# Kernel tuning notes

Hardware: AMD Instinct MI355X
Metric: run time of the kernel (lower is better)

The kernel has to match this reference:

```python
import jax, jax.numpy as jnp
import numpy as np

APP_DIM = 27
FEA_PE = 6
VIEW_PE = 6
FEATURE_C = 128
DENSITY_SHIFT = -10.0
DISTANCE_SCALE = 25.0
IN_MLPC = 2 * VIEW_PE * 3 + 2 * FEA_PE * APP_DIM + 3 + APP_DIM  # 390


def positional_encoding(x, freqs):
    # x: [..., C] -> [..., 2*freqs*C]
    freq_bands = (2.0 ** jnp.arange(freqs)).astype(x.dtype)
    pts = (x[..., None] * freq_bands).reshape(x.shape[:-1] + (freqs * x.shape[-1],))
    return jnp.concatenate([jnp.sin(pts), jnp.cos(pts)], axis=-1)


def alpha2weights(alpha):
    # alpha: [N_rays, N_samples]; last sample forced opaque (as in source)
    alpha = alpha.at[:, -1].set(1.0)
    trans = jnp.concatenate(
        [jnp.ones((alpha.shape[0], 1), alpha.dtype), 1.0 - alpha + 1e-10], axis=-1)
    T = jnp.cumprod(trans, axis=-1)
    weights = alpha * T[:, :-1]
    return weights, T


def setup_inputs() -> dict:
    key = jax.random.key(0)
    ks = jax.random.split(key, 12)
    N_rays, N_samples = 4096, 128
    sigma_feat = jax.random.normal(ks[0], (N_rays, N_samples), jnp.float32)
    app_features = 0.1 * jax.random.normal(ks[1], (N_rays, N_samples, APP_DIM), jnp.float32)
    vd = jax.random.normal(ks[2], (N_rays, N_samples, 3), jnp.float32)
    viewdirs = vd / (jnp.linalg.norm(vd, axis=-1, keepdims=True) + 1e-8)
    dists = 0.02 * jax.random.uniform(ks[3], (N_rays, N_samples), jnp.float32)

    def linear(k, fan_in, fan_out):
        kw, kb = jax.random.split(k)
        lim = 1.0 / np.sqrt(fan_in)
        W = jax.random.uniform(kw, (fan_in, fan_out), jnp.float32, -lim, lim)
        b = jax.random.uniform(kb, (fan_out,), jnp.float32, -lim, lim)
        return W, b

    W1, b1 = linear(ks[4], IN_MLPC, FEATURE_C)
    W2, b2 = linear(ks[5], FEATURE_C, FEATURE_C)
    W3, _ = linear(ks[6], FEATURE_C, 3)
    b3 = jnp.zeros((3,), jnp.float32)  # bias of last layer initialized to 0 in source
    return {"sigma_feat": sigma_feat, "app_features": app_features,
            "viewdirs": viewdirs, "dists": dists,
            "W1": W1, "b1": b1, "W2": W2, "b2": b2, "W3": W3, "b3": b3}


def reference(sigma_feat, app_features, viewdirs, dists, W1, b1, W2, b2, W3, b3):
    # feature2density: softplus with density_shift
    sigma = jax.nn.softplus(sigma_feat + DENSITY_SHIFT)
    alpha = 1.0 - jnp.exp(-sigma * dists * DISTANCE_SCALE)  # [N_rays, N_samples]
    weights, _T = alpha2weights(alpha)

    # MLPRender_Fea: cat[features, viewdirs, PE(features), PE(viewdirs)]
    mlp_in = jnp.concatenate(
        [app_features, viewdirs,
         positional_encoding(app_features, FEA_PE),
         positional_encoding(viewdirs, VIEW_PE)], axis=-1)  # [R, S, 390]
    h = jax.nn.relu(jnp.einsum('rsc,cf->rsf', mlp_in, W1) + b1)
    h = jax.nn.relu(jnp.einsum('rsf,fg->rsg', h, W2) + b2)
    rgb = jax.nn.sigmoid(jnp.einsum('rsg,go->rso', h, W3) + b3)  # [R, S, 3]

    rgb_map = jnp.sum(weights[..., None] * rgb, axis=-2)  # [R, 3]
    return rgb_map
```

## Files before the change

kernel.cpp:

```cpp
#include <hip/hip_runtime.h>
#include <math.h>

typedef unsigned short u16;
using bf16x8 = __attribute__((ext_vector_type(8))) short;
using f32x4  = __attribute__((ext_vector_type(4))) float;

#define NS      128
#define NBLOCKS 4096
#define KS1     15
#define NSLICE  19

#define POOLSZ 16384

#define BAR() do { asm volatile("s_waitcnt lgkmcnt(0)" ::: "memory");        \
                   __builtin_amdgcn_s_barrier();                              \
                   asm volatile("" ::: "memory"); } while (0)

#define MF(A,B,C) __builtin_amdgcn_mfma_f32_16x16x32_bf16((A),(B),(C),0,0,0)

__device__ __forceinline__ u16 f2bf(float f) {
    unsigned int i = __float_as_uint(f);
    return (u16)((i + 0x7FFFu + ((i >> 16) & 1u)) >> 16);
}

__device__ __forceinline__ unsigned pk(float hi, float lo) {
    unsigned r;
    asm("v_cvt_pk_bf16_f32 %0, %1, %2" : "=v"(r) : "v"(lo), "v"(hi));
    return r;
}
__device__ __forceinline__ u16 f2bf1(float f) {
    return (u16)((__float_as_uint(f) + 0x8000u) >> 16);
}

__device__ __forceinline__ int afoff_h(int m, int k) {
    int chunk = ((k >> 5) * 8 + (m >> 4)) * 64 + ((k >> 3) & 3) * 16 + (m & 15);
    chunk ^= (k >> 3) & 3;
    return chunk * 8 + (k & 7);
}

__device__ __forceinline__ int orig_k(int ch, int slot) {
    if (ch < 27) {
        if (slot == 0) return ch;
        if (slot <= 6) return 30 + ch * 6 + (slot - 1);
        return 192 + ch * 6 + (slot - 7);
    } else {
        int c = ch - 27;
        if (slot == 0) return 27 + c;
        if (slot <= 6) return 354 + c * 6 + (slot - 1);
        return 372 + c * 6 + (slot - 7);
    }
}

__device__ __forceinline__ float ldch(const float* ap, const float* vp, int c) {
    return (c < 27) ? ap[c] : vp[c - 27];
}

__device__ __forceinline__ void build_x(u16* Xb, int m_b, int cl_b, float v) {
    float rev = v * 0.15915494309189535f;
    rev -= floorf(rev);
    float s0 = __builtin_amdgcn_sinf(rev);
    float c0 = __builtin_amdgcn_cosf(rev);
    float s1 = 2.f * s0 * c0, c1 = c0 * c0 - s0 * s0;
    float s2 = 2.f * s1 * c1, c2 = c1 * c1 - s1 * s1;
    float s3 = 2.f * s2 * c2, c3 = c2 * c2 - s2 * s2;
    float s4 = 2.f * s3 * c3, c4 = c3 * c3 - s3 * s3;
    float s5 = 2.f * s4 * c4, c5 = c4 * c4 - s4 * s4;
    uint4 lo, hi;
    lo.x = pk(s0, v);  lo.y = pk(s2, s1);  lo.z = pk(s4, s3);  lo.w = pk(c0, s5);
    hi.x = pk(c2, c1); hi.y = pk(c4, c3);  hi.z = pk(0.f, c5); hi.w = 0u;
    int base = (m_b >> 4) * 512 + ((2 * cl_b) * 16 + (m_b & 15)) * 8;
    *(uint4*)(Xb + base)       = lo;
    *(uint4*)(Xb + base + 128) = hi;
}

__global__ __launch_bounds__(256) void prep_kernel(
    const float* __restrict__ W1, const float* __restrict__ W2,
    const float* __restrict__ W3, u16* __restrict__ ws)
{
    int idx = blockIdx.x * 256 + threadIdx.x;
    if (idx < 61440) {
        int j = idx & 7, lane = (idx >> 3) & 63, nt = (idx >> 9) & 7, ks = idx >> 12;
        int q = lane >> 4, l15 = lane & 15;
        int klocal = q * 8 + j;
        int ch = ks * 2 + (klocal >> 4);
        int slot = klocal & 15;
        int n = nt * 16 + l15;
        ws[idx] = (slot < 13) ? f2bf(W1[orig_k(ch, slot) * 128 + n]) : (u16)0;
    } else if (idx < 77824) {
        int i2 = idx - 61440;
        int j = i2 & 7, lane = (i2 >> 3) & 63, nt = (i2 >> 9) & 7, ks = i2 >> 12;
        int k = ks * 32 + (lane >> 4) * 8 + j;
        int n = nt * 16 + (lane & 15);
        ws[idx] = f2bf(W2[k * 128 + n]);
    } else if (idx < 79872) {
        int i3 = idx - 77824;
        int j = i3 & 7, lane = (i3 >> 3) & 63, ks = i3 >> 9;
        int k = ks * 32 + (lane >> 4) * 8 + j;
        int n = lane & 15;
        ws[idx] = (n < 3) ? f2bf(W3[k * 3 + n]) : (u16)0;
    }
}

#define PHASE(g, BC0,BC1,BC2,BC3, BN0,BN1,BN2,BN3)                            \
  {                                                                           \
    const u16* wpn = wp0 + (2*(g)+2) * 4096;          \
    BN0 = *(const bf16x8*)(wpn);                                              \
    BN1 = *(const bf16x8*)(wpn + 512);                                        \
    BN2 = *(const bf16x8*)(wpn + 4096);                                       \
    BN3 = *(const bf16x8*)(wpn + 4096 + 512);                                 \
    if (4*((g)+2) + cl < 30)                         \
        pv_nxt = ldch(ap, vp, 4*((g)+2) + cl);                                \
    const u16* ab = pool + ((((g)&1) ? 8192 : 0)) + (wm*256 + lane)*8;        \
    bf16x8 a0 = *(const bf16x8*)(ab);                                         \
    bf16x8 a1 = *(const bf16x8*)(ab + 512);                                   \
    bf16x8 a2 = *(const bf16x8*)(ab + 1024);                                  \
    bf16x8 a3 = *(const bf16x8*)(ab + 1536);                                  \
    acc[0][0]=MF(a0,BC0,acc[0][0]); acc[0][1]=MF(a0,BC1,acc[0][1]);           \
    acc[1][0]=MF(a1,BC0,acc[1][0]); acc[1][1]=MF(a1,BC1,acc[1][1]);           \
    acc[2][0]=MF(a2,BC0,acc[2][0]); acc[2][1]=MF(a2,BC1,acc[2][1]);           \
    acc[3][0]=MF(a3,BC0,acc[3][0]); acc[3][1]=MF(a3,BC1,acc[3][1]);           \
    a0 = *(const bf16x8*)(ab + 4096);                                         \
    a1 = *(const bf16x8*)(ab + 4096 + 512);                                   \
    a2 = *(const bf16x8*)(ab + 4096 + 1024);                                  \
    a3 = *(const bf16x8*)(ab + 4096 + 1536);                                  \
    acc[0][0]=MF(a0,BC2,acc[0][0]); acc[0][1]=MF(a0,BC3,acc[0][1]);           \
    acc[1][0]=MF(a1,BC2,acc[1][0]); acc[1][1]=MF(a1,BC3,acc[1][1]);           \
    acc[2][0]=MF(a2,BC2,acc[2][0]); acc[2][1]=MF(a2,BC3,acc[2][1]);           \
    acc[3][0]=MF(a3,BC2,acc[3][0]); acc[3][1]=MF(a3,BC3,acc[3][1]);           \
    if (4*((g)+1) + cl < 30)                             \
        build_x(pool + ((((g)+1)&1) ? 8192 : 0) + (cl>>1)*4096, row, cl&1,    \
                pv_cur);                                                      \
    pv_cur = pv_nxt;                                                          \
    BAR();                                                                    \
  }

__global__ __launch_bounds__(512, 4) void render_kernel(
    const float* __restrict__ sigma_g, const float* __restrict__ app_g,
    const float* __restrict__ view_g,  const float* __restrict__ dists_g,
    const float* __restrict__ b1_g,    const float* __restrict__ b2_g,
    const float* __restrict__ b3_g,    const u16* __restrict__ ws,
    float* __restrict__ out_g)
{
    __shared__ __align__(16) u16 pool[POOLSZ];
    __shared__ __align__(16) float part[NS * 3];
    __shared__ float scanS;
    __shared__ float sum2[6];

    const int tid  = threadIdx.x;
    const int lane = tid & 63;
    const int wave = tid >> 6;
    const int l15  = lane & 15;
    const int quad = lane >> 4;
    const int wm   = wave >> 2;
    const int wn   = wave & 3;

    const int r  = blockIdx.x;
    const int rb = r * NS;
    const int row = tid & 127;
    const int cl  = tid >> 7;
    const float* ap = app_g  + (rb + row) * 27;
    const float* vp = view_g + (rb + row) * 3;

    const u16* wp0 = ws + (wn * 128 + lane) * 8;
    bf16x8 bP0, bP1, bP2, bP3, bQ0, bQ1, bQ2, bQ3;
    bP0 = *(const bf16x8*)(wp0);
    bP1 = *(const bf16x8*)(wp0 + 512);
    bP2 = *(const bf16x8*)(wp0 + 4096);
    bP3 = *(const bf16x8*)(wp0 + 4096 + 512);

    const float b1r0 = b1_g[wn * 32 + l15];
    const float b1r1 = b1_g[wn * 32 + 16 + l15];

    float pv_cur = ldch(ap, vp, cl);
    float pv_nxt = ldch(ap, vp, 4 + cl);

    float alpha = 0.f, prod = 1.f, wr = 0.f;
    if (tid < NS) {
        float x  = sigma_g[rb + tid] - 10.f;
        float sp = (x > 20.f) ? x : log1pf(expf(x));
        alpha = 1.f - expf(-sp * dists_g[rb + tid] * 25.f);
        if (tid == NS - 1) alpha = 1.f;
        float tb = 1.f - alpha + 1e-10f;
        prod = tb;
        #pragma unroll
        for (int d = 1; d < 64; d <<= 1) {
            float v = __shfl_up(prod, d);
            if (lane >= d) prod *= v;
        }
        if (tid == 63) scanS = prod;
    }

    build_x(pool + (cl >> 1) * 4096, row, cl & 1, pv_cur);
    pv_cur = pv_nxt;
    BAR();

    if (tid < NS) {
        float prev = __shfl_up(prod, 1);
        float base = (lane == 0) ? 1.f : prev;
        float scale = (wave == 1) ? scanS : 1.f;
        wr = alpha * base * scale;
    }

    const f32x4 vzero = {0.f, 0.f, 0.f, 0.f};
    f32x4 acc[4][2];
    #pragma unroll
    for (int mt = 0; mt < 4; ++mt)
        #pragma unroll
        for (int nt = 0; nt < 2; ++nt) acc[mt][nt] = vzero;

    #pragma unroll 1
    for (int t = 0; t < 3; ++t) {
        PHASE(2 * t,     bP0, bP1, bP2, bP3, bQ0, bQ1, bQ2, bQ3);
        PHASE(2 * t + 1, bQ0, bQ1, bQ2, bQ3, bP0, bP1, bP2, bP3);
    }
    PHASE(6, bP0, bP1, bP2, bP3, bQ0, bQ1, bQ2, bQ3);

    {
        const u16* wpn = wp0 + 16 * 4096;
        bf16x8 w2a0 = *(const bf16x8*)(wpn);
        bf16x8 w2a1 = *(const bf16x8*)(wpn + 512);
        bf16x8 w2b0 = *(const bf16x8*)(wpn + 4096);
        bf16x8 w2b1 = *(const bf16x8*)(wpn + 4096 + 512);
        bf16x8 w2c0 = *(const bf16x8*)(wpn + 8192);
        bf16x8 w2c1 = *(const bf16x8*)(wpn + 8192 + 512);

        const u16* ab = pool + 8192 + (wm * 256 + lane) * 8;
        bf16x8 a0 = *(const bf16x8*)(ab);
        bf16x8 a1 = *(const bf16x8*)(ab + 512);
        bf16x8 a2 = *(const bf16x8*)(ab + 1024);
        bf16x8 a3 = *(const bf16x8*)(ab + 1536);
        acc[0][0]=MF(a0,bQ0,acc[0][0]); acc[0][1]=MF(a0,bQ1,acc[0][1]);
        acc[1][0]=MF(a1,bQ0,acc[1][0]); acc[1][1]=MF(a1,bQ1,acc[1][1]);
        acc[2][0]=MF(a2,bQ0,acc[2][0]); acc[2][1]=MF(a2,bQ1,acc[2][1]);
        acc[3][0]=MF(a3,bQ0,acc[3][0]); acc[3][1]=MF(a3,bQ1,acc[3][1]);
        BAR();

        #pragma unroll
        for (int mt = 0; mt < 4; ++mt)
            #pragma unroll
            for (int nt = 0; nt < 2; ++nt) {
                int col = wn * 32 + nt * 16 + l15;
                #pragma unroll
                for (int rr = 0; rr < 4; ++rr) {
                    int rw = wm * 64 + mt * 16 + quad * 4 + rr;
                    pool[afoff_h(rw, col)] =
                        f2bf1(fmaxf(acc[mt][nt][rr] + ((nt == 0) ? b1r0 : b1r1), 0.f));
                }
                acc[mt][nt] = vzero;
            }
        BAR();

        #define G2(ks, B0, B1)                                                \
          {                                                                   \
            int cb = ((ks) * 512 + wm * 256 + lane) ^ quad;                   \
            bf16x8 h0 = *(const bf16x8*)(pool + cb * 8);                      \
            bf16x8 h1v = *(const bf16x8*)(pool + (cb + 64) * 8);              \
            bf16x8 h2v = *(const bf16x8*)(pool + (cb + 128) * 8);             \
            bf16x8 h3v = *(const bf16x8*)(pool + (cb + 192) * 8);             \
            acc[0][0]=MF(h0,B0,acc[0][0]); acc[0][1]=MF(h0,B1,acc[0][1]);     \
            acc[1][0]=MF(h1v,B0,acc[1][0]); acc[1][1]=MF(h1v,B1,acc[1][1]);   \
            acc[2][0]=MF(h2v,B0,acc[2][0]); acc[2][1]=MF(h2v,B1,acc[2][1]);   \
            acc[3][0]=MF(h3v,B0,acc[3][0]); acc[3][1]=MF(h3v,B1,acc[3][1]);   \
          }
        G2(0, bQ2, bQ3);
        G2(1, w2a0, w2a1);
        G2(2, w2b0, w2b1);
        G2(3, w2c0, w2c1);
        #undef G2
        BAR();
    }

    const float b2r0 = b2_g[wn * 32 + l15];
    const float b2r1 = b2_g[wn * 32 + 16 + l15];
    #pragma unroll
    for (int mt = 0; mt < 4; ++mt)
        #pragma unroll
        for (int nt = 0; nt < 2; ++nt) {
            int col = wn * 32 + nt * 16 + l15;
            #pragma unroll
            for (int rr = 0; rr < 4; ++rr) {
                int rw = wm * 64 + mt * 16 + quad * 4 + rr;
                pool[afoff_h(rw, col)] =
                    f2bf1(fmaxf(acc[mt][nt][rr] + ((nt == 0) ? b2r0 : b2r1), 0.f));
            }
        }
    BAR();

    const u16* w3r = ws + 77824;
    const float b3v = (l15 < 3) ? b3_g[l15] : 0.f;
    f32x4 acc3 = vzero;
    #pragma unroll
    for (int ks = 0; ks < 4; ++ks) {
        bf16x8 w3f = *(const bf16x8*)(w3r + (ks * 64 + lane) * 8);
        int c = ((ks * 8 + wave) * 64 + lane) ^ quad;
        bf16x8 a3 = *(const bf16x8*)(pool + c * 8);
        acc3 = MF(a3, w3f, acc3);
    }
    if (l15 < 3) {
        #pragma unroll
        for (int rr = 0; rr < 4; ++rr) {
            int rw = wave * 16 + quad * 4 + rr;
            float v = acc3[rr] + b3v;
            part[rw * 3 + l15] = 1.f / (1.f + expf(-v));
        }
    }
    BAR();

    if (tid < NS) {
        float v0 = wr * part[tid * 3 + 0];
        float v1 = wr * part[tid * 3 + 1];
        float v2 = wr * part[tid * 3 + 2];
        #pragma unroll
        for (int d = 1; d < 64; d <<= 1) {
            v0 += __shfl_xor(v0, d);
            v1 += __shfl_xor(v1, d);
            v2 += __shfl_xor(v2, d);
        }
        if (lane == 0) {
            sum2[wave * 3 + 0] = v0;
            sum2[wave * 3 + 1] = v1;
            sum2[wave * 3 + 2] = v2;
        }
    }
    BAR();
    if (tid == 0) {
        out_g[r * 3 + 0] = sum2[0] + sum2[3];
        out_g[r * 3 + 1] = sum2[1] + sum2[4];
        out_g[r * 3 + 2] = sum2[2] + sum2[5];
    }
}

extern "C" void kernel_launch(void* const* d_in, const int* in_sizes, int n_in,
                              void* d_out, int out_size, void* d_ws, size_t ws_size,
                              hipStream_t stream) {
    (void)in_sizes; (void)n_in; (void)out_size; (void)ws_size;
    const float* sigma = (const float*)d_in[0];
    const float* app   = (const float*)d_in[1];
    const float* view  = (const float*)d_in[2];
    const float* dists = (const float*)d_in[3];
    const float* W1    = (const float*)d_in[4];
    const float* b1    = (const float*)d_in[5];
    const float* W2    = (const float*)d_in[6];
    const float* b2    = (const float*)d_in[7];
    const float* W3    = (const float*)d_in[8];
    const float* b3    = (const float*)d_in[9];
    float* out = (float*)d_out;

    u16* ws = (u16*)d_ws;

    prep_kernel<<<312, 256, 0, stream>>>(W1, W2, W3, ws);
    render_kernel<<<NBLOCKS, 512, 0, stream>>>(sigma, app, view, dists,
                                               b1, b2, b3, ws, out);
}
```

Measured before the change: 206.7 us.

## Retile MLP waves to 4x2 grid with triple-buffered weight prefetch and MFMA priority

```diff
diff --git a/kernel.cpp b/kernel.cpp
--- a/kernel.cpp
+++ b/kernel.cpp
@@ -101,36 +101,51 @@
     }
 }
 
-#define PHASE(g, BC0,BC1,BC2,BC3, BN0,BN1,BN2,BN3)                            \
+#define LOADB(N0,N1,N2,N3, s)                                                 \
+    if ((s) < NSLICE) {                                                       \
+        const u16* wp = wp0 + (s) * 4096;                                     \
+        N0 = *(const bf16x8*)(wp);                                            \
+        N1 = *(const bf16x8*)(wp + 512);                                      \
+        N2 = *(const bf16x8*)(wp + 1024);                                     \
+        N3 = *(const bf16x8*)(wp + 1536);                                     \
+    }
+
+#define BODYX(s, C0,C1,C2,C3, N0,N1,N2,N3)                                    \
   {                                                                           \
-    const u16* wpn = wp0 + (2*(g)+2) * 4096;          \
-    BN0 = *(const bf16x8*)(wpn);                                              \
-    BN1 = *(const bf16x8*)(wpn + 512);                                        \
-    BN2 = *(const bf16x8*)(wpn + 4096);                                       \
-    BN3 = *(const bf16x8*)(wpn + 4096 + 512);                                 \
-    if (4*((g)+2) + cl < 30)                         \
-        pv_nxt = ldch(ap, vp, 4*((g)+2) + cl);                                \
-    const u16* ab = pool + ((((g)&1) ? 8192 : 0)) + (wm*256 + lane)*8;        \
+    LOADB(N0,N1,N2,N3, (s)+2);                                                \
+    const u16* ab = pool + ((((s)>>1)&1) ? 8192 : 0) + (((s)&1)*4096)         \
+                    + (wm*128 + lane)*8;                                      \
     bf16x8 a0 = *(const bf16x8*)(ab);                                         \
     bf16x8 a1 = *(const bf16x8*)(ab + 512);                                   \
-    bf16x8 a2 = *(const bf16x8*)(ab + 1024);                                  \
-    bf16x8 a3 = *(const bf16x8*)(ab + 1536);                                  \
-    acc[0][0]=MF(a0,BC0,acc[0][0]); acc[0][1]=MF(a0,BC1,acc[0][1]);           \
-    acc[1][0]=MF(a1,BC0,acc[1][0]); acc[1][1]=MF(a1,BC1,acc[1][1]);           \
-    acc[2][0]=MF(a2,BC0,acc[2][0]); acc[2][1]=MF(a2,BC1,acc[2][1]);           \
-    acc[3][0]=MF(a3,BC0,acc[3][0]); acc[3][1]=MF(a3,BC1,acc[3][1]);           \
-    a0 = *(const bf16x8*)(ab + 4096);                                         \
-    a1 = *(const bf16x8*)(ab + 4096 + 512);                                   \
-    a2 = *(const bf16x8*)(ab + 4096 + 1024);                                  \
-    a3 = *(const bf16x8*)(ab + 4096 + 1536);                                  \
-    acc[0][0]=MF(a0,BC2,acc[0][0]); acc[0][1]=MF(a0,BC3,acc[0][1]);           \
-    acc[1][0]=MF(a1,BC2,acc[1][0]); acc[1][1]=MF(a1,BC3,acc[1][1]);           \
-    acc[2][0]=MF(a2,BC2,acc[2][0]); acc[2][1]=MF(a2,BC3,acc[2][1]);           \
-    acc[3][0]=MF(a3,BC2,acc[3][0]); acc[3][1]=MF(a3,BC3,acc[3][1]);           \
-    if (4*((g)+1) + cl < 30)                             \
+    __builtin_amdgcn_s_setprio(1);                                            \
+    acc[0][0]=MF(a0,C0,acc[0][0]); acc[0][1]=MF(a0,C1,acc[0][1]);             \
+    acc[0][2]=MF(a0,C2,acc[0][2]); acc[0][3]=MF(a0,C3,acc[0][3]);             \
+    acc[1][0]=MF(a1,C0,acc[1][0]); acc[1][1]=MF(a1,C1,acc[1][1]);             \
+    acc[1][2]=MF(a1,C2,acc[1][2]); acc[1][3]=MF(a1,C3,acc[1][3]);             \
+    __builtin_amdgcn_s_setprio(0);                                            \
+  }
+
+#define BODYH(s, C0,C1,C2,C3, N0,N1,N2,N3)                                    \
+  {                                                                           \
+    LOADB(N0,N1,N2,N3, (s)+2);                                                \
+    int cb0 = ((((s)-15)*512) + wm*128 + lane) ^ quad;                        \
+    bf16x8 a0 = *(const bf16x8*)(pool + cb0*8);                               \
+    bf16x8 a1 = *(const bf16x8*)(pool + (cb0+64)*8);                          \
+    __builtin_amdgcn_s_setprio(1);                                            \
+    acc[0][0]=MF(a0,C0,acc[0][0]); acc[0][1]=MF(a0,C1,acc[0][1]);             \
+    acc[0][2]=MF(a0,C2,acc[0][2]); acc[0][3]=MF(a0,C3,acc[0][3]);             \
+    acc[1][0]=MF(a1,C0,acc[1][0]); acc[1][1]=MF(a1,C1,acc[1][1]);             \
+    acc[1][2]=MF(a1,C2,acc[1][2]); acc[1][3]=MF(a1,C3,acc[1][3]);             \
+    __builtin_amdgcn_s_setprio(0);                                            \
+  }
+
+#define GEND(g)                                                               \
+  {                                                                           \
+    if (4*((g)+3) + cl < 30) pv_nxt2 = ldch(ap, vp, 4*((g)+3) + cl);          \
+    if (4*((g)+1) + cl < 30)                                                  \
         build_x(pool + ((((g)+1)&1) ? 8192 : 0) + (cl>>1)*4096, row, cl&1,    \
                 pv_cur);                                                      \
-    pv_cur = pv_nxt;                                                          \
+    pv_cur = pv_nxt; pv_nxt = pv_nxt2;                                        \
     BAR();                                                                    \
   }
 
@@ -151,8 +166,8 @@
     const int wave = tid >> 6;
     const int l15  = lane & 15;
     const int quad = lane >> 4;
-    const int wm   = wave >> 2;
-    const int wn   = wave & 3;
+    const int wm   = wave >> 1;
+    const int wn   = wave & 1;
 
     const int r  = blockIdx.x;
     const int rb = r * NS;
@@ -161,18 +176,18 @@
     const float* ap = app_g  + (rb + row) * 27;
     const float* vp = view_g + (rb + row) * 3;
 
-    const u16* wp0 = ws + (wn * 128 + lane) * 8;
-    bf16x8 bP0, bP1, bP2, bP3, bQ0, bQ1, bQ2, bQ3;
-    bP0 = *(const bf16x8*)(wp0);
-    bP1 = *(const bf16x8*)(wp0 + 512);
-    bP2 = *(const bf16x8*)(wp0 + 4096);
-    bP3 = *(const bf16x8*)(wp0 + 4096 + 512);
-
-    const float b1r0 = b1_g[wn * 32 + l15];
-    const float b1r1 = b1_g[wn * 32 + 16 + l15];
-
-    float pv_cur = ldch(ap, vp, cl);
-    float pv_nxt = ldch(ap, vp, 4 + cl);
+    const u16* wp0 = ws + wn * 2048 + lane * 8;
+    bf16x8 bP0, bP1, bP2, bP3, bQ0, bQ1, bQ2, bQ3, bR0, bR1, bR2, bR3;
+    LOADB(bP0, bP1, bP2, bP3, 0);
+    LOADB(bQ0, bQ1, bQ2, bQ3, 1);
+
+    float b1r[4];
+    #pragma unroll
+    for (int nt = 0; nt < 4; ++nt) b1r[nt] = b1_g[wn * 64 + nt * 16 + l15];
+
+    float pv_cur  = ldch(ap, vp, cl);
+    float pv_nxt  = ldch(ap, vp, 4 + cl);
+    float pv_nxt2 = ldch(ap, vp, 8 + cl);
 
     float alpha = 0.f, prod = 1.f, wr = 0.f;
     if (tid < NS) {
@@ -191,7 +206,7 @@
     }
 
     build_x(pool + (cl >> 1) * 4096, row, cl & 1, pv_cur);
-    pv_cur = pv_nxt;
+    pv_cur = pv_nxt; pv_nxt = pv_nxt2;
     BAR();
 
     if (tid < NS) {
@@ -202,86 +217,63 @@
     }
 
     const f32x4 vzero = {0.f, 0.f, 0.f, 0.f};
-    f32x4 acc[4][2];
-    #pragma unroll
-    for (int mt = 0; mt < 4; ++mt)
-        #pragma unroll
-        for (int nt = 0; nt < 2; ++nt) acc[mt][nt] = vzero;
-
-    #pragma unroll 1
-    for (int t = 0; t < 3; ++t) {
-        PHASE(2 * t,     bP0, bP1, bP2, bP3, bQ0, bQ1, bQ2, bQ3);
-        PHASE(2 * t + 1, bQ0, bQ1, bQ2, bQ3, bP0, bP1, bP2, bP3);
-    }
-    PHASE(6, bP0, bP1, bP2, bP3, bQ0, bQ1, bQ2, bQ3);
-
-    {
-        const u16* wpn = wp0 + 16 * 4096;
-        bf16x8 w2a0 = *(const bf16x8*)(wpn);
-        bf16x8 w2a1 = *(const bf16x8*)(wpn + 512);
-        bf16x8 w2b0 = *(const bf16x8*)(wpn + 4096);
-        bf16x8 w2b1 = *(const bf16x8*)(wpn + 4096 + 512);
-        bf16x8 w2c0 = *(const bf16x8*)(wpn + 8192);
-        bf16x8 w2c1 = *(const bf16x8*)(wpn + 8192 + 512);
-
-        const u16* ab = pool + 8192 + (wm * 256 + lane) * 8;
-        bf16x8 a0 = *(const bf16x8*)(ab);
-        bf16x8 a1 = *(const bf16x8*)(ab + 512);
-        bf16x8 a2 = *(const bf16x8*)(ab + 1024);
-        bf16x8 a3 = *(const bf16x8*)(ab + 1536);
-        acc[0][0]=MF(a0,bQ0,acc[0][0]); acc[0][1]=MF(a0,bQ1,acc[0][1]);
-        acc[1][0]=MF(a1,bQ0,acc[1][0]); acc[1][1]=MF(a1,bQ1,acc[1][1]);
-        acc[2][0]=MF(a2,bQ0,acc[2][0]); acc[2][1]=MF(a2,bQ1,acc[2][1]);
-        acc[3][0]=MF(a3,bQ0,acc[3][0]); acc[3][1]=MF(a3,bQ1,acc[3][1]);
-        BAR();
-
-        #pragma unroll
-        for (int mt = 0; mt < 4; ++mt)
-            #pragma unroll
-            for (int nt = 0; nt < 2; ++nt) {
-                int col = wn * 32 + nt * 16 + l15;
-                #pragma unroll
-                for (int rr = 0; rr < 4; ++rr) {
-                    int rw = wm * 64 + mt * 16 + quad * 4 + rr;
-                    pool[afoff_h(rw, col)] =
-                        f2bf1(fmaxf(acc[mt][nt][rr] + ((nt == 0) ? b1r0 : b1r1), 0.f));
-                }
-                acc[mt][nt] = vzero;
-            }
-        BAR();
-
-        #define G2(ks, B0, B1)                                                \
-          {                                                                   \
-            int cb = ((ks) * 512 + wm * 256 + lane) ^ quad;                   \
-            bf16x8 h0 = *(const bf16x8*)(pool + cb * 8);                      \
-            bf16x8 h1v = *(const bf16x8*)(pool + (cb + 64) * 8);              \
-            bf16x8 h2v = *(const bf16x8*)(pool + (cb + 128) * 8);             \
-            bf16x8 h3v = *(const bf16x8*)(pool + (cb + 192) * 8);             \
-            acc[0][0]=MF(h0,B0,acc[0][0]); acc[0][1]=MF(h0,B1,acc[0][1]);     \
-            acc[1][0]=MF(h1v,B0,acc[1][0]); acc[1][1]=MF(h1v,B1,acc[1][1]);   \
-            acc[2][0]=MF(h2v,B0,acc[2][0]); acc[2][1]=MF(h2v,B1,acc[2][1]);   \
-            acc[3][0]=MF(h3v,B0,acc[3][0]); acc[3][1]=MF(h3v,B1,acc[3][1]);   \
-          }
-        G2(0, bQ2, bQ3);
-        G2(1, w2a0, w2a1);
-        G2(2, w2b0, w2b1);
-        G2(3, w2c0, w2c1);
-        #undef G2
-        BAR();
-    }
-
-    const float b2r0 = b2_g[wn * 32 + l15];
-    const float b2r1 = b2_g[wn * 32 + 16 + l15];
-    #pragma unroll
-    for (int mt = 0; mt < 4; ++mt)
-        #pragma unroll
-        for (int nt = 0; nt < 2; ++nt) {
-            int col = wn * 32 + nt * 16 + l15;
+    f32x4 acc[2][4];
+    #pragma unroll
+    for (int mt = 0; mt < 2; ++mt)
+        #pragma unroll
+        for (int nt = 0; nt < 4; ++nt) acc[mt][nt] = vzero;
+
+    BODYX(0,  bP0,bP1,bP2,bP3, bR0,bR1,bR2,bR3);
+    BODYX(1,  bQ0,bQ1,bQ2,bQ3, bP0,bP1,bP2,bP3);  GEND(0);
+    BODYX(2,  bR0,bR1,bR2,bR3, bQ0,bQ1,bQ2,bQ3);
+    BODYX(3,  bP0,bP1,bP2,bP3, bR0,bR1,bR2,bR3);  GEND(1);
+    BODYX(4,  bQ0,bQ1,bQ2,bQ3, bP0,bP1,bP2,bP3);
+    BODYX(5,  bR0,bR1,bR2,bR3, bQ0,bQ1,bQ2,bQ3);  GEND(2);
+    BODYX(6,  bP0,bP1,bP2,bP3, bR0,bR1,bR2,bR3);
+    BODYX(7,  bQ0,bQ1,bQ2,bQ3, bP0,bP1,bP2,bP3);  GEND(3);
+    BODYX(8,  bR0,bR1,bR2,bR3, bQ0,bQ1,bQ2,bQ3);
+    BODYX(9,  bP0,bP1,bP2,bP3, bR0,bR1,bR2,bR3);  GEND(4);
+    BODYX(10, bQ0,bQ1,bQ2,bQ3, bP0,bP1,bP2,bP3);
+    BODYX(11, bR0,bR1,bR2,bR3, bQ0,bQ1,bQ2,bQ3);  GEND(5);
+    BODYX(12, bP0,bP1,bP2,bP3, bR0,bR1,bR2,bR3);
+    BODYX(13, bQ0,bQ1,bQ2,bQ3, bP0,bP1,bP2,bP3);  GEND(6);
+    BODYX(14, bR0,bR1,bR2,bR3, bQ0,bQ1,bQ2,bQ3);
+    BAR();
+
+    #pragma unroll
+    for (int mt = 0; mt < 2; ++mt)
+        #pragma unroll
+        for (int nt = 0; nt < 4; ++nt) {
+            int col = wn * 64 + nt * 16 + l15;
             #pragma unroll
             for (int rr = 0; rr < 4; ++rr) {
-                int rw = wm * 64 + mt * 16 + quad * 4 + rr;
+                int rw = wm * 32 + mt * 16 + quad * 4 + rr;
                 pool[afoff_h(rw, col)] =
-                    f2bf1(fmaxf(acc[mt][nt][rr] + ((nt == 0) ? b2r0 : b2r1), 0.f));
+                    f2bf1(fmaxf(acc[mt][nt][rr] + b1r[nt], 0.f));
+            }
+            acc[mt][nt] = vzero;
+        }
+    BAR();
+
+    BODYH(15, bP0,bP1,bP2,bP3, bR0,bR1,bR2,bR3);
+    BODYH(16, bQ0,bQ1,bQ2,bQ3, bP0,bP1,bP2,bP3);
+    BODYH(17, bR0,bR1,bR2,bR3, bQ0,bQ1,bQ2,bQ3);
+    BODYH(18, bP0,bP1,bP2,bP3, bR0,bR1,bR2,bR3);
+    BAR();
+
+    float b2r[4];
+    #pragma unroll
+    for (int nt = 0; nt < 4; ++nt) b2r[nt] = b2_g[wn * 64 + nt * 16 + l15];
+    #pragma unroll
+    for (int mt = 0; mt < 2; ++mt)
+        #pragma unroll
+        for (int nt = 0; nt < 4; ++nt) {
+            int col = wn * 64 + nt * 16 + l15;
+            #pragma unroll
+            for (int rr = 0; rr < 4; ++rr) {
+                int rw = wm * 32 + mt * 16 + quad * 4 + rr;
+                pool[afoff_h(rw, col)] =
+                    f2bf1(fmaxf(acc[mt][nt][rr] + b2r[nt], 0.f));
             }
         }
     BAR();
```

Result: slower. 217.4 us (+5.2%).

## Fully unroll slice pipeline with 3-deep B prefetch and raise occupancy bound

Applied to the files above, without the earlier changes.

```diff
diff --git a/kernel.cpp b/kernel.cpp
--- a/kernel.cpp
+++ b/kernel.cpp
@@ -55,7 +55,7 @@
     return (c < 27) ? ap[c] : vp[c - 27];
 }
 
-__device__ __forceinline__ void build_x(u16* Xb, int m_b, int cl_b, float v) {
+__device__ __forceinline__ void build_x(u16* dst, float v) {
     float rev = v * 0.15915494309189535f;
     rev -= floorf(rev);
     float s0 = __builtin_amdgcn_sinf(rev);
@@ -68,9 +68,8 @@
     uint4 lo, hi;
     lo.x = pk(s0, v);  lo.y = pk(s2, s1);  lo.z = pk(s4, s3);  lo.w = pk(c0, s5);
     hi.x = pk(c2, c1); hi.y = pk(c4, c3);  hi.z = pk(0.f, c5); hi.w = 0u;
-    int base = (m_b >> 4) * 512 + ((2 * cl_b) * 16 + (m_b & 15)) * 8;
-    *(uint4*)(Xb + base)       = lo;
-    *(uint4*)(Xb + base + 128) = hi;
+    *(uint4*)(dst)       = lo;
+    *(uint4*)(dst + 128) = hi;
 }
 
 __global__ __launch_bounds__(256) void prep_kernel(
@@ -101,40 +100,57 @@
     }
 }
 
-#define PHASE(g, BC0,BC1,BC2,BC3, BN0,BN1,BN2,BN3)                            \
+#define LOADB2(N0, N1, s)                                                     \
+    if ((s) < NSLICE) {                                                       \
+        const u16* wp = wp0 + (s) * 4096;                                     \
+        N0 = *(const bf16x8*)(wp);                                            \
+        N1 = *(const bf16x8*)(wp + 512);                                      \
+    }
+
+#define BODYX(s, C0,C1, N0,N1)                                                \
   {                                                                           \
-    const u16* wpn = wp0 + (2*(g)+2) * 4096;          \
-    BN0 = *(const bf16x8*)(wpn);                                              \
-    BN1 = *(const bf16x8*)(wpn + 512);                                        \
-    BN2 = *(const bf16x8*)(wpn + 4096);                                       \
-    BN3 = *(const bf16x8*)(wpn + 4096 + 512);                                 \
-    if (4*((g)+2) + cl < 30)                         \
-        pv_nxt = ldch(ap, vp, 4*((g)+2) + cl);                                \
-    const u16* ab = pool + ((((g)&1) ? 8192 : 0)) + (wm*256 + lane)*8;        \
+    LOADB2(N0, N1, (s)+2);                                                    \
+    const u16* ab = pool + ((((s)>>1)&1) ? 8192 : 0) + (((s)&1)*4096)         \
+                    + (wm*256 + lane)*8;                                      \
     bf16x8 a0 = *(const bf16x8*)(ab);                                         \
     bf16x8 a1 = *(const bf16x8*)(ab + 512);                                   \
-    bf16x8 a2 = *(const bf16x8*)(ab + 1024);                                  \
-    bf16x8 a3 = *(const bf16x8*)(ab + 1536);                                  \
-    acc[0][0]=MF(a0,BC0,acc[0][0]); acc[0][1]=MF(a0,BC1,acc[0][1]);           \
-    acc[1][0]=MF(a1,BC0,acc[1][0]); acc[1][1]=MF(a1,BC1,acc[1][1]);           \
-    acc[2][0]=MF(a2,BC0,acc[2][0]); acc[2][1]=MF(a2,BC1,acc[2][1]);           \
-    acc[3][0]=MF(a3,BC0,acc[3][0]); acc[3][1]=MF(a3,BC1,acc[3][1]);           \
-    a0 = *(const bf16x8*)(ab + 4096);                                         \
-    a1 = *(const bf16x8*)(ab + 4096 + 512);                                   \
-    a2 = *(const bf16x8*)(ab + 4096 + 1024);                                  \
-    a3 = *(const bf16x8*)(ab + 4096 + 1536);                                  \
-    acc[0][0]=MF(a0,BC2,acc[0][0]); acc[0][1]=MF(a0,BC3,acc[0][1]);           \
-    acc[1][0]=MF(a1,BC2,acc[1][0]); acc[1][1]=MF(a1,BC3,acc[1][1]);           \
-    acc[2][0]=MF(a2,BC2,acc[2][0]); acc[2][1]=MF(a2,BC3,acc[2][1]);           \
-    acc[3][0]=MF(a3,BC2,acc[3][0]); acc[3][1]=MF(a3,BC3,acc[3][1]);           \
-    if (4*((g)+1) + cl < 30)                             \
-        build_x(pool + ((((g)+1)&1) ? 8192 : 0) + (cl>>1)*4096, row, cl&1,    \
+    __builtin_amdgcn_s_setprio(1);                                            \
+    acc[0][0]=MF(a0,C0,acc[0][0]); acc[0][1]=MF(a0,C1,acc[0][1]);             \
+    acc[1][0]=MF(a1,C0,acc[1][0]); acc[1][1]=MF(a1,C1,acc[1][1]);             \
+    a0 = *(const bf16x8*)(ab + 1024);                                         \
+    a1 = *(const bf16x8*)(ab + 1536);                                         \
+    acc[2][0]=MF(a0,C0,acc[2][0]); acc[2][1]=MF(a0,C1,acc[2][1]);             \
+    acc[3][0]=MF(a1,C0,acc[3][0]); acc[3][1]=MF(a1,C1,acc[3][1]);             \
+    __builtin_amdgcn_s_setprio(0);                                            \
+  }
+
+#define BODYH(s, C0,C1, N0,N1)                                                \
+  {                                                                           \
+    LOADB2(N0, N1, (s)+2);                                                    \
+    int cb = ((((s)-15)*512) + wm*256 + lane) ^ quad;                         \
+    bf16x8 a0 = *(const bf16x8*)(pool + cb*8);                                \
+    bf16x8 a1 = *(const bf16x8*)(pool + (cb+64)*8);                           \
+    __builtin_amdgcn_s_setprio(1);                                            \
+    acc[0][0]=MF(a0,C0,acc[0][0]); acc[0][1]=MF(a0,C1,acc[0][1]);             \
+    acc[1][0]=MF(a1,C0,acc[1][0]); acc[1][1]=MF(a1,C1,acc[1][1]);             \
+    a0 = *(const bf16x8*)(pool + (cb+128)*8);                                 \
+    a1 = *(const bf16x8*)(pool + (cb+192)*8);                                 \
+    acc[2][0]=MF(a0,C0,acc[2][0]); acc[2][1]=MF(a0,C1,acc[2][1]);             \
+    acc[3][0]=MF(a1,C0,acc[3][0]); acc[3][1]=MF(a1,C1,acc[3][1]);             \
+    __builtin_amdgcn_s_setprio(0);                                            \
+  }
+
+#define GEND(g)                                                               \
+  {                                                                           \
+    if (4*((g)+1) + cl < 30)                                                  \
+        build_x(pool + ((((g)+1)&1) ? 8192 : 0) + (cl>>1)*4096 + bxoff,       \
                 pv_cur);                                                      \
     pv_cur = pv_nxt;                                                          \
+    if (4*((g)+3) + cl < 30) pv_nxt = ldch(ap, vp, 4*((g)+3) + cl);           \
     BAR();                                                                    \
   }
 
-__global__ __launch_bounds__(512, 4) void render_kernel(
+__global__ __launch_bounds__(512, 6) void render_kernel(
     const float* __restrict__ sigma_g, const float* __restrict__ app_g,
     const float* __restrict__ view_g,  const float* __restrict__ dists_g,
     const float* __restrict__ b1_g,    const float* __restrict__ b2_g,
@@ -160,16 +176,12 @@
     const int cl  = tid >> 7;
     const float* ap = app_g  + (rb + row) * 27;
     const float* vp = view_g + (rb + row) * 3;
+    const int bxoff = (row >> 4) * 512 + (((cl & 1) * 32) + (row & 15)) * 8;
 
     const u16* wp0 = ws + (wn * 128 + lane) * 8;
-    bf16x8 bP0, bP1, bP2, bP3, bQ0, bQ1, bQ2, bQ3;
-    bP0 = *(const bf16x8*)(wp0);
-    bP1 = *(const bf16x8*)(wp0 + 512);
-    bP2 = *(const bf16x8*)(wp0 + 4096);
-    bP3 = *(const bf16x8*)(wp0 + 4096 + 512);
-
-    const float b1r0 = b1_g[wn * 32 + l15];
-    const float b1r1 = b1_g[wn * 32 + 16 + l15];
+    bf16x8 bP0, bP1, bQ0, bQ1, bR0, bR1;
+    LOADB2(bP0, bP1, 0);
+    LOADB2(bQ0, bQ1, 1);
 
     float pv_cur = ldch(ap, vp, cl);
     float pv_nxt = ldch(ap, vp, 4 + cl);
@@ -190,8 +202,9 @@
         if (tid == 63) scanS = prod;
     }
 
-    build_x(pool + (cl >> 1) * 4096, row, cl & 1, pv_cur);
+    build_x(pool + (cl >> 1) * 4096 + bxoff, pv_cur);
     pv_cur = pv_nxt;
+    pv_nxt = ldch(ap, vp, 8 + cl);
     BAR();
 
     if (tid < NS) {
@@ -208,67 +221,45 @@
         #pragma unroll
         for (int nt = 0; nt < 2; ++nt) acc[mt][nt] = vzero;
 
-    #pragma unroll 1
-    for (int t = 0; t < 3; ++t) {
-        PHASE(2 * t,     bP0, bP1, bP2, bP3, bQ0, bQ1, bQ2, bQ3);
-        PHASE(2 * t + 1, bQ0, bQ1, bQ2, bQ3, bP0, bP1, bP2, bP3);
-    }
-    PHASE(6, bP0, bP1, bP2, bP3, bQ0, bQ1, bQ2, bQ3);
-
-    {
-        const u16* wpn = wp0 + 16 * 4096;
-        bf16x8 w2a0 = *(const bf16x8*)(wpn);
-        bf16x8 w2a1 = *(const bf16x8*)(wpn + 512);
-        bf16x8 w2b0 = *(const bf16x8*)(wpn + 4096);
-        bf16x8 w2b1 = *(const bf16x8*)(wpn + 4096 + 512);
-        bf16x8 w2c0 = *(const bf16x8*)(wpn + 8192);
-        bf16x8 w2c1 = *(const bf16x8*)(wpn + 8192 + 512);
-
-        const u16* ab = pool + 8192 + (wm * 256 + lane) * 8;
-        bf16x8 a0 = *(const bf16x8*)(ab);
-        bf16x8 a1 = *(const bf16x8*)(ab + 512);
-        bf16x8 a2 = *(const bf16x8*)(ab + 1024);
-        bf16x8 a3 = *(const bf16x8*)(ab + 1536);
-        acc[0][0]=MF(a0,bQ0,acc[0][0]); acc[0][1]=MF(a0,bQ1,acc[0][1]);
-        acc[1][0]=MF(a1,bQ0,acc[1][0]); acc[1][1]=MF(a1,bQ1,acc[1][1]);
-        acc[2][0]=MF(a2,bQ0,acc[2][0]); acc[2][1]=MF(a2,bQ1,acc[2][1]);
-        acc[3][0]=MF(a3,bQ0,acc[3][0]); acc[3][1]=MF(a3,bQ1,acc[3][1]);
-        BAR();
-
-        #pragma unroll
-        for (int mt = 0; mt < 4; ++mt)
+    BODYX(0,  bP0,bP1, bR0,bR1);
+    BODYX(1,  bQ0,bQ1, bP0,bP1);  GEND(0);
+    BODYX(2,  bR0,bR1, bQ0,bQ1);
+    BODYX(3,  bP0,bP1, bR0,bR1);  GEND(1);
+    BODYX(4,  bQ0,bQ1, bP0,bP1);
+    BODYX(5,  bR0,bR1, bQ0,bQ1);  GEND(2);
+    BODYX(6,  bP0,bP1, bR0,bR1);
+    BODYX(7,  bQ0,bQ1, bP0,bP1);  GEND(3);
+    BODYX(8,  bR0,bR1, bQ0,bQ1);
+    BODYX(9,  bP0,bP1, bR0,bR1);  GEND(4);
+    BODYX(10, bQ0,bQ1, bP0,bP1);
+    BODYX(11, bR0,bR1, bQ0,bQ1);  GEND(5);
+    BODYX(12, bP0,bP1, bR0,bR1);
+    BODYX(13, bQ0,bQ1, bP0,bP1);  GEND(6);
+    BODYX(14, bR0,bR1, bQ0,bQ1);
+    const float b1r0 = b1_g[wn * 32 + l15];
+    const float b1r1 = b1_g[wn * 32 + 16 + l15];
+    BAR();
+
+    #pragma unroll
+    for (int mt = 0; mt < 4; ++mt)
+        #pragma unroll
+        for (int nt = 0; nt < 2; ++nt) {
+            int col = wn * 32 + nt * 16 + l15;
             #pragma unroll
-            for (int nt = 0; nt < 2; ++nt) {
-                int col = wn * 32 + nt * 16 + l15;
-                #pragma unroll
-                for (int rr = 0; rr < 4; ++rr) {
-                    int rw = wm * 64 + mt * 16 + quad * 4 + rr;
-                    pool[afoff_h(rw, col)] =
-                        f2bf1(fmaxf(acc[mt][nt][rr] + ((nt == 0) ? b1r0 : b1r1), 0.f));
-                }
-                acc[mt][nt] = vzero;
+            for (int rr = 0; rr < 4; ++rr) {
+                int rw = wm * 64 + mt * 16 + quad * 4 + rr;
+                pool[afoff_h(rw, col)] =
+                    f2bf1(fmaxf(acc[mt][nt][rr] + ((nt == 0) ? b1r0 : b1r1), 0.f));
             }
-        BAR();
-
-        #define G2(ks, B0, B1)                                                \
-          {                                                                   \
-            int cb = ((ks) * 512 + wm * 256 + lane) ^ quad;                   \
-            bf16x8 h0 = *(const bf16x8*)(pool + cb * 8);                      \
-            bf16x8 h1v = *(const bf16x8*)(pool + (cb + 64) * 8);              \
-            bf16x8 h2v = *(const bf16x8*)(pool + (cb + 128) * 8);             \
-            bf16x8 h3v = *(const bf16x8*)(pool + (cb + 192) * 8);             \
-            acc[0][0]=MF(h0,B0,acc[0][0]); acc[0][1]=MF(h0,B1,acc[0][1]);     \
-            acc[1][0]=MF(h1v,B0,acc[1][0]); acc[1][1]=MF(h1v,B1,acc[1][1]);   \
-            acc[2][0]=MF(h2v,B0,acc[2][0]); acc[2][1]=MF(h2v,B1,acc[2][1]);   \
-            acc[3][0]=MF(h3v,B0,acc[3][0]); acc[3][1]=MF(h3v,B1,acc[3][1]);   \
-          }
-        G2(0, bQ2, bQ3);
-        G2(1, w2a0, w2a1);
-        G2(2, w2b0, w2b1);
-        G2(3, w2c0, w2c1);
-        #undef G2
-        BAR();
-    }
+            acc[mt][nt] = vzero;
+        }
+    BAR();
+
+    BODYH(15, bP0,bP1, bR0,bR1);
+    BODYH(16, bQ0,bQ1, bP0,bP1);
+    BODYH(17, bR0,bR1, bQ0,bQ1);
+    BODYH(18, bP0,bP1, bR0,bR1);
+    BAR();
 
     const float b2r0 = b2_g[wn * 32 + l15];
     const float b2r1 = b2_g[wn * 32 + 16 + l15];
```

After: 418.4 us. 102% more time.
